# Kernel tuning notes

Hardware: AMD Instinct MI355X
Metric: run time of the kernel (lower is better)

## Reference

```python
import jax, jax.numpy as jnp
import numpy as np
from jax import lax

FILTERS = 256
KERNEL = 1
BATCH, T, D = 16, 2048, 512


def conv1d_same(x, w, b):
    # x: [B, T, Cin], w: [K, Cin, Cout], b: [Cout]
    y = lax.conv_general_dilated(
        x, w, window_strides=(1,), padding='SAME',
        dimension_numbers=('NWC', 'WIO', 'NWC'))
    return y + b


def setup_inputs() -> dict:
    key = jax.random.key(0)
    ks = jax.random.split(key, 5)
    inputs = jax.random.normal(ks[0], (BATCH, T, D), dtype=jnp.float32)
    # Glorot-ish init for conv kernels
    W_qkv = jax.random.normal(ks[1], (KERNEL, D, 3 * FILTERS), dtype=jnp.float32) * (1.0 / np.sqrt(D))
    b_qkv = jnp.zeros((3 * FILTERS,), dtype=jnp.float32)
    W_out = jax.random.normal(ks[2], (KERNEL, FILTERS, D), dtype=jnp.float32) * (1.0 / np.sqrt(FILTERS))
    b_out = jnp.zeros((D,), dtype=jnp.float32)
    return {"inputs": inputs, "W_qkv": W_qkv, "b_qkv": b_qkv, "W_out": W_out, "b_out": b_out}


def reference(inputs, W_qkv, b_qkv, W_out, b_out):
    # QKV projection: conv1d(kernel=1) == pointwise linear, kept general via conv
    qkv = conv1d_same(inputs, W_qkv, b_qkv)          # [B, T, 3F]
    q, k, v = jnp.split(qkv, 3, axis=-1)             # each [B, T, F]
    scale = jnp.sqrt(jnp.asarray(FILTERS, dtype=q.dtype))
    score = jnp.einsum('btf,bsf->bts', q, k) / scale  # [B, T, T]
    attn = jax.nn.softmax(score, axis=-1)
    context = jnp.einsum('bts,bsf->btf', attn, v)    # [B, T, F]
    output = conv1d_same(context, W_out, b_out)      # [B, T, D]
    return inputs + output
```

## Files before the change

kernel.cpp:

```cpp
#include <hip/hip_runtime.h>

typedef __bf16 bf16_t;
typedef __attribute__((ext_vector_type(8))) __bf16 bf16x8;
typedef __attribute__((ext_vector_type(4))) __bf16 bf16x4;
typedef __attribute__((ext_vector_type(4))) float f32x4;

#define GLL16(gsrc, ldst)                                                                   \
  __builtin_amdgcn_global_load_lds(                                                         \
      (const __attribute__((address_space(1))) unsigned int*)(gsrc),                        \
      (__attribute__((address_space(3))) unsigned int*)(ldst), 16, 0, 0)

#define BATCH 16
#define TT    2048
#define DD    512
#define FF    256
#define MTOT  (BATCH * TT)

__global__ __launch_bounds__(256) void cast_x_kernel(const float* __restrict__ x,
                                                     bf16_t* __restrict__ xb, int n4) {
  int stride = gridDim.x * blockDim.x;
  for (int i = blockIdx.x * blockDim.x + threadIdx.x; i < n4; i += stride) {
    float4 v = ((const float4*)x)[i];
    bf16x4 o;
    o[0] = (bf16_t)v.x; o[1] = (bf16_t)v.y; o[2] = (bf16_t)v.z; o[3] = (bf16_t)v.w;
    ((bf16x4*)xb)[i] = o;
  }
}

__global__ __launch_bounds__(256) void cast_w_kernel(const float* __restrict__ Wqkv,
                                                     const float* __restrict__ Wout,
                                                     bf16_t* __restrict__ WqkvT,
                                                     bf16_t* __restrict__ WoutT) {
  int t = blockIdx.x * blockDim.x + threadIdx.x;
  if (t < 768 * 512) {
    int n = t >> 9, k = t & 511;
    WqkvT[t] = (bf16_t)Wqkv[k * 768 + n];
  } else {
    int t2 = t - 768 * 512;
    if (t2 < 512 * 256) {
      int n = t2 >> 8, k = t2 & 255;
      WoutT[t2] = (bf16_t)Wout[k * 512 + n];
    }
  }
}

__global__ __launch_bounds__(256) void gemm_qkv_kernel(const bf16_t* __restrict__ A,
                                                       const bf16_t* __restrict__ Bt,
                                                       const float* __restrict__ bias,
                                                       bf16_t* __restrict__ Qo,
                                                       bf16_t* __restrict__ Ko,
                                                       bf16_t* __restrict__ Vt) {
  __shared__ __align__(16) bf16_t Al[2][128 * 32];
  __shared__ __align__(16) bf16_t Bl[2][128 * 32];
  const int tid = threadIdx.x;
  const int l = tid & 63, w = tid >> 6;
  const int g = l >> 4, r = l & 15;
  const int wm = w >> 1, wn = w & 1;
  const int m0 = blockIdx.y * 128;
  const int n0 = blockIdx.x * 128;
  const int lda = 512, ldb = 512;
  const bf16_t* Abase = A + (size_t)m0 * lda;
  const bf16_t* Bbase = Bt + (size_t)n0 * ldb;

  f32x4 acc[4][4] = {};

  auto stage = [&](int kt, int bufi) {
    const int k0 = kt * 32;
#pragma unroll
    for (int rnd = 0; rnd < 2; ++rnd) {
      int idx = rnd * 256 + tid;
      int row = idx >> 2, d = idx & 3;
      int sc = d ^ ((row >> 1) & 3);
      GLL16(Abase + row * lda + k0 + sc * 8, &Al[bufi][idx * 8]);
    }
#pragma unroll
    for (int rnd = 0; rnd < 2; ++rnd) {
      int idx = rnd * 256 + tid;
      int row = idx >> 2, d = idx & 3;
      int sc = d ^ ((row >> 1) & 3);
      GLL16(Bbase + row * ldb + k0 + sc * 8, &Bl[bufi][idx * 8]);
    }
  };

  stage(0, 0);
  __syncthreads();
  int buf = 0;
  const int NK = 512 / 32;
  for (int kt = 0; kt < NK; ++kt) {
    if (kt + 1 < NK) stage(kt + 1, buf ^ 1);
    bf16x8 af[4], bfr[4];
#pragma unroll
    for (int mi = 0; mi < 4; ++mi) {
      int row = wm * 64 + mi * 16 + r;
      int cc = g ^ ((row >> 1) & 3);
      af[mi] = *(const bf16x8*)&Al[buf][row * 32 + cc * 8];
    }
#pragma unroll
    for (int ni = 0; ni < 4; ++ni) {
      int row = wn * 64 + ni * 16 + r;
      int cc = g ^ ((row >> 1) & 3);
      bfr[ni] = *(const bf16x8*)&Bl[buf][row * 32 + cc * 8];
    }
#pragma unroll
    for (int mi = 0; mi < 4; ++mi)
#pragma unroll
      for (int ni = 0; ni < 4; ++ni)
        acc[mi][ni] = __builtin_amdgcn_mfma_f32_16x16x32_bf16(af[mi], bfr[ni], acc[mi][ni], 0, 0, 0);
    __syncthreads();
    buf ^= 1;
  }

  const int qsel = n0 >> 8;
#pragma unroll
  for (int mi = 0; mi < 4; ++mi) {
    int row0 = m0 + wm * 64 + mi * 16 + g * 4;
#pragma unroll
    for (int ni = 0; ni < 4; ++ni) {
      int col = n0 + wn * 64 + ni * 16 + r;
      float bv = bias[col];
      int cl = col & 255;
      if (qsel == 2) {
        bf16x4 pk;
#pragma unroll
        for (int i = 0; i < 4; ++i) pk[i] = (bf16_t)(acc[mi][ni][i] + bv);
        int b = row0 >> 11, t0 = row0 & 2047;
        *(bf16x4*)&Vt[((size_t)(b * 256 + cl)) * 2048 + t0] = pk;
      } else {
        bf16_t* dst = (qsel == 0) ? Qo : Ko;
#pragma unroll
        for (int i = 0; i < 4; ++i)
          dst[(size_t)(row0 + i) * 256 + cl] = (bf16_t)(acc[mi][ni][i] + bv);
      }
    }
  }
}

__global__ __launch_bounds__(512, 2) void attn_kernel(const bf16_t* __restrict__ Q,
                                                      const bf16_t* __restrict__ K,
                                                      const bf16_t* __restrict__ Vt,
                                                      bf16_t* __restrict__ ctx) {
  __shared__ __align__(16) bf16_t Kl[64 * 256];
  __shared__ __align__(16) bf16_t Vl[256 * 64];
  __shared__ __align__(16) bf16_t Pl[8][16 * 72];
  const int tid = threadIdx.x;
  const int l = tid & 63, w = tid >> 6;
  const int g = l >> 4, r = l & 15;
  const int b = blockIdx.y;
  const int q0 = blockIdx.x * 128 + w * 16;
  const bf16_t* Kb = K + ((size_t)b * TT) * 256;
  const bf16_t* Vb = Vt + (size_t)b * 256 * TT;

  bf16x8 qf[8];
  const bf16_t* Qrow = Q + ((size_t)(b * TT) + q0 + r) * 256;
#pragma unroll
  for (int kf = 0; kf < 8; ++kf) qf[kf] = *(const bf16x8*)(Qrow + kf * 32 + g * 8);

  f32x4 cacc[16] = {};
  float m_run = -3.0e38f, l_run = 0.0f;

  for (int kv0 = 0; kv0 < TT; kv0 += 64) {
    __syncthreads();
#pragma unroll
    for (int rnd = 0; rnd < 4; ++rnd) {
      int idx = rnd * 512 + tid;
      int row = idx >> 5, d = idx & 31;
      int sc = d ^ (row & 7);
      GLL16(Kb + (size_t)(kv0 + row) * 256 + sc * 8, &Kl[idx * 8]);
    }
#pragma unroll
    for (int rnd = 0; rnd < 4; ++rnd) {
      int idx = rnd * 512 + tid;
      int row = idx >> 3, d = idx & 7;
      int sc = d ^ (row & 7);
      GLL16(Vb + (size_t)row * TT + kv0 + sc * 8, &Vl[idx * 8]);
    }
    __syncthreads();

    f32x4 st[4] = {};
#pragma unroll
    for (int kf = 0; kf < 8; ++kf) {
#pragma unroll
      for (int kvf = 0; kvf < 4; ++kvf) {
        int row = kvf * 16 + r;
        int c = kf * 4 + g;
        bf16x8 kfr = *(const bf16x8*)&Kl[row * 256 + ((c ^ (row & 7)) * 8)];
        st[kvf] = __builtin_amdgcn_mfma_f32_16x16x32_bf16(kfr, qf[kf], st[kvf], 0, 0, 0);
      }
    }

    float tmax = -3.0e38f;
    float s[4][4];
#pragma unroll
    for (int kvf = 0; kvf < 4; ++kvf)
#pragma unroll
      for (int i = 0; i < 4; ++i) {
        s[kvf][i] = st[kvf][i] * 0.0625f;
        tmax = fmaxf(tmax, s[kvf][i]);
      }
    tmax = fmaxf(tmax, __shfl_xor(tmax, 16));
    tmax = fmaxf(tmax, __shfl_xor(tmax, 32));
    float mnew = fmaxf(m_run, tmax);
    float alpha = __expf(m_run - mnew);
    float psum = 0.0f;
#pragma unroll
    for (int kvf = 0; kvf < 4; ++kvf) {
      bf16x4 pk;
#pragma unroll
      for (int i = 0; i < 4; ++i) {
        float p = __expf(s[kvf][i] - mnew);
        psum += p;
        pk[i] = (bf16_t)p;
      }
      *(bf16x4*)&Pl[w][r * 72 + kvf * 16 + g * 4] = pk;
    }
    psum += __shfl_xor(psum, 16);
    psum += __shfl_xor(psum, 32);
    l_run = l_run * alpha + psum;
    m_run = mnew;
#pragma unroll
    for (int fc = 0; fc < 16; ++fc)
#pragma unroll
      for (int i = 0; i < 4; ++i) cacc[fc][i] *= alpha;

#pragma unroll
    for (int kk = 0; kk < 2; ++kk) {
      bf16x8 pf = *(const bf16x8*)&Pl[w][r * 72 + kk * 32 + g * 8];
#pragma unroll
      for (int fc = 0; fc < 16; ++fc) {
        int row = fc * 16 + r;
        int c = kk * 4 + g;
        bf16x8 vf = *(const bf16x8*)&Vl[row * 64 + ((c ^ (row & 7)) * 8)];
        cacc[fc] = __builtin_amdgcn_mfma_f32_16x16x32_bf16(vf, pf, cacc[fc], 0, 0, 0);
      }
    }
  }

  float inv = 1.0f / l_run;
  bf16_t* crow = ctx + ((size_t)(b * TT) + q0 + r) * 256;
#pragma unroll
  for (int fc = 0; fc < 16; ++fc) {
    bf16x4 pk;
#pragma unroll
    for (int i = 0; i < 4; ++i) pk[i] = (bf16_t)(cacc[fc][i] * inv);
    *(bf16x4*)(crow + fc * 16 + g * 4) = pk;
  }
}

__global__ __launch_bounds__(256) void gemm_out_kernel(const bf16_t* __restrict__ A,
                                                       const bf16_t* __restrict__ Bt,
                                                       const float* __restrict__ bias,
                                                       const float* __restrict__ X,
                                                       float* __restrict__ Out) {
  __shared__ __align__(16) bf16_t Al[2][128 * 32];
  __shared__ __align__(16) bf16_t Bl[2][128 * 32];
  const int tid = threadIdx.x;
  const int l = tid & 63, w = tid >> 6;
  const int g = l >> 4, r = l & 15;
  const int wm = w >> 1, wn = w & 1;
  const int m0 = blockIdx.y * 128;
  const int n0 = blockIdx.x * 128;
  const int lda = 256, ldb = 256;
  const bf16_t* Abase = A + (size_t)m0 * lda;
  const bf16_t* Bbase = Bt + (size_t)n0 * ldb;

  f32x4 acc[4][4] = {};

  auto stage = [&](int kt, int bufi) {
    const int k0 = kt * 32;
#pragma unroll
    for (int rnd = 0; rnd < 2; ++rnd) {
      int idx = rnd * 256 + tid;
      int row = idx >> 2, d = idx & 3;
      int sc = d ^ ((row >> 1) & 3);
      GLL16(Abase + row * lda + k0 + sc * 8, &Al[bufi][idx * 8]);
    }
#pragma unroll
    for (int rnd = 0; rnd < 2; ++rnd) {
      int idx = rnd * 256 + tid;
      int row = idx >> 2, d = idx & 3;
      int sc = d ^ ((row >> 1) & 3);
      GLL16(Bbase + row * ldb + k0 + sc * 8, &Bl[bufi][idx * 8]);
    }
  };

  stage(0, 0);
  __syncthreads();
  int buf = 0;
  const int NK = 256 / 32;
  for (int kt = 0; kt < NK; ++kt) {
    if (kt + 1 < NK) stage(kt + 1, buf ^ 1);
    bf16x8 af[4], bfr[4];
#pragma unroll
    for (int mi = 0; mi < 4; ++mi) {
      int row = wm * 64 + mi * 16 + r;
      int cc = g ^ ((row >> 1) & 3);
      af[mi] = *(const bf16x8*)&Al[buf][row * 32 + cc * 8];
    }
#pragma unroll
    for (int ni = 0; ni < 4; ++ni) {
      int row = wn * 64 + ni * 16 + r;
      int cc = g ^ ((row >> 1) & 3);
      bfr[ni] = *(const bf16x8*)&Bl[buf][row * 32 + cc * 8];
    }
#pragma unroll
    for (int mi = 0; mi < 4; ++mi)
#pragma unroll
      for (int ni = 0; ni < 4; ++ni)
        acc[mi][ni] = __builtin_amdgcn_mfma_f32_16x16x32_bf16(af[mi], bfr[ni], acc[mi][ni], 0, 0, 0);
    __syncthreads();
    buf ^= 1;
  }

#pragma unroll
  for (int mi = 0; mi < 4; ++mi) {
    int row0 = m0 + wm * 64 + mi * 16 + g * 4;
#pragma unroll
    for (int ni = 0; ni < 4; ++ni) {
      int col = n0 + wn * 64 + ni * 16 + r;
      float bv = bias[col];
#pragma unroll
      for (int i = 0; i < 4; ++i) {
        size_t off = (size_t)(row0 + i) * 512 + col;
        Out[off] = acc[mi][ni][i] + bv + X[off];
      }
    }
  }
}

extern "C" void kernel_launch(void* const* d_in, const int* in_sizes, int n_in,
                              void* d_out, int out_size, void* d_ws, size_t ws_size,
                              hipStream_t stream) {
  const float* X    = (const float*)d_in[0];
  const float* Wqkv = (const float*)d_in[1];
  const float* bqkv = (const float*)d_in[2];
  const float* Wout = (const float*)d_in[3];
  const float* bout = (const float*)d_in[4];
  float* out = (float*)d_out;

  char* ws = (char*)d_ws;
  bf16_t* Xbf   = (bf16_t*)ws;
  bf16_t* ctx   = Xbf;
  bf16_t* WqkvT = (bf16_t*)(ws + 33554432);
  bf16_t* WoutT = (bf16_t*)(ws + 34340864);
  bf16_t* Qb    = (bf16_t*)(ws + 34603008);
  bf16_t* Kb    = (bf16_t*)(ws + 51380224);
  bf16_t* Vt    = (bf16_t*)(ws + 68157440);

  cast_x_kernel<<<2048, 256, 0, stream>>>(X, Xbf, (MTOT * DD) / 4);
  cast_w_kernel<<<2048, 256, 0, stream>>>(Wqkv, Wout, WqkvT, WoutT);
  gemm_qkv_kernel<<<dim3(6, 256), 256, 0, stream>>>(Xbf, WqkvT, bqkv, Qb, Kb, Vt);
  attn_kernel<<<dim3(16, 16), 512, 0, stream>>>(Qb, Kb, Vt, ctx);
  gemm_out_kernel<<<dim3(4, 256), 256, 0, stream>>>(ctx, WoutT, bout, X, out);
}
```

Baseline: 334.2 us.

## Double-buffer attention K/V loads, lazy softmax rescale, XCD-aware block remap

```diff
diff --git a/kernel.cpp b/kernel.cpp
--- a/kernel.cpp
+++ b/kernel.cpp
@@ -56,8 +56,10 @@
   const int l = tid & 63, w = tid >> 6;
   const int g = l >> 4, r = l & 15;
   const int wm = w >> 1, wn = w & 1;
-  const int m0 = blockIdx.y * 128;
-  const int n0 = blockIdx.x * 128;
+  const int lin = blockIdx.x;
+  const int wid = (lin & 7) * 192 + (lin >> 3);
+  const int m0 = (wid / 6) * 128;
+  const int n0 = (wid % 6) * 128;
   const int lda = 512, ldb = 512;
   const bf16_t* Abase = A + (size_t)m0 * lda;
   const bf16_t* Bbase = Bt + (size_t)n0 * ldb;
@@ -139,14 +141,16 @@
                                                       const bf16_t* __restrict__ K,
                                                       const bf16_t* __restrict__ Vt,
                                                       bf16_t* __restrict__ ctx) {
-  __shared__ __align__(16) bf16_t Kl[64 * 256];
-  __shared__ __align__(16) bf16_t Vl[256 * 64];
-  __shared__ __align__(16) bf16_t Pl[8][16 * 72];
+  __shared__ __align__(16) bf16_t Kl[2][64 * 256];
+  __shared__ __align__(16) bf16_t Vl[2][256 * 64];
+  __shared__ __align__(16) bf16_t Pl[8][16 * 64];
   const int tid = threadIdx.x;
   const int l = tid & 63, w = tid >> 6;
   const int g = l >> 4, r = l & 15;
-  const int b = blockIdx.y;
-  const int q0 = blockIdx.x * 128 + w * 16;
+  const int lin = blockIdx.x;
+  const int wid = (lin & 7) * 32 + (lin >> 3);
+  const int b = wid >> 4;
+  const int q0 = (wid & 15) * 128 + w * 16;
   const bf16_t* Kb = K + ((size_t)b * TT) * 256;
   const bf16_t* Vb = Vt + (size_t)b * 256 * TT;
 
@@ -158,23 +162,29 @@
   f32x4 cacc[16] = {};
   float m_run = -3.0e38f, l_run = 0.0f;
 
-  for (int kv0 = 0; kv0 < TT; kv0 += 64) {
-    __syncthreads();
+  auto stage = [&](int kv0, int bi) {
 #pragma unroll
     for (int rnd = 0; rnd < 4; ++rnd) {
       int idx = rnd * 512 + tid;
       int row = idx >> 5, d = idx & 31;
       int sc = d ^ (row & 7);
-      GLL16(Kb + (size_t)(kv0 + row) * 256 + sc * 8, &Kl[idx * 8]);
+      GLL16(Kb + (size_t)(kv0 + row) * 256 + sc * 8, &Kl[bi][idx * 8]);
     }
 #pragma unroll
     for (int rnd = 0; rnd < 4; ++rnd) {
       int idx = rnd * 512 + tid;
       int row = idx >> 3, d = idx & 7;
       int sc = d ^ (row & 7);
-      GLL16(Vb + (size_t)row * TT + kv0 + sc * 8, &Vl[idx * 8]);
-    }
-    __syncthreads();
+      GLL16(Vb + (size_t)row * TT + kv0 + sc * 8, &Vl[bi][idx * 8]);
+    }
+  };
+
+  stage(0, 0);
+  __syncthreads();
+  int buf = 0;
+
+  for (int kv0 = 0; kv0 < TT; kv0 += 64) {
+    if (kv0 + 64 < TT) stage(kv0 + 64, buf ^ 1);
 
     f32x4 st[4] = {};
 #pragma unroll
@@ -183,7 +193,7 @@
       for (int kvf = 0; kvf < 4; ++kvf) {
         int row = kvf * 16 + r;
         int c = kf * 4 + g;
-        bf16x8 kfr = *(const bf16x8*)&Kl[row * 256 + ((c ^ (row & 7)) * 8)];
+        bf16x8 kfr = *(const bf16x8*)&Kl[buf][row * 256 + ((c ^ (row & 7)) * 8)];
         st[kvf] = __builtin_amdgcn_mfma_f32_16x16x32_bf16(kfr, qf[kf], st[kvf], 0, 0, 0);
       }
     }
@@ -199,40 +209,47 @@
       }
     tmax = fmaxf(tmax, __shfl_xor(tmax, 16));
     tmax = fmaxf(tmax, __shfl_xor(tmax, 32));
-    float mnew = fmaxf(m_run, tmax);
-    float alpha = __expf(m_run - mnew);
+    if (!__all(tmax - m_run <= 8.0f)) {
+      float mnew = fmaxf(m_run, tmax);
+      float alpha = __expf(m_run - mnew);
+      l_run *= alpha;
+#pragma unroll
+      for (int fc = 0; fc < 16; ++fc)
+#pragma unroll
+        for (int i = 0; i < 4; ++i) cacc[fc][i] *= alpha;
+      m_run = mnew;
+    }
     float psum = 0.0f;
 #pragma unroll
     for (int kvf = 0; kvf < 4; ++kvf) {
       bf16x4 pk;
 #pragma unroll
       for (int i = 0; i < 4; ++i) {
-        float p = __expf(s[kvf][i] - mnew);
+        float p = __expf(s[kvf][i] - m_run);
         psum += p;
         pk[i] = (bf16_t)p;
       }
-      *(bf16x4*)&Pl[w][r * 72 + kvf * 16 + g * 4] = pk;
+      int widx = r * 64 + ((((kvf * 2 + (g >> 1)) ^ (r & 7)) << 3) | ((g & 1) * 4));
+      *(bf16x4*)&Pl[w][widx] = pk;
     }
     psum += __shfl_xor(psum, 16);
     psum += __shfl_xor(psum, 32);
-    l_run = l_run * alpha + psum;
-    m_run = mnew;
-#pragma unroll
-    for (int fc = 0; fc < 16; ++fc)
-#pragma unroll
-      for (int i = 0; i < 4; ++i) cacc[fc][i] *= alpha;
+    l_run += psum;
 
 #pragma unroll
     for (int kk = 0; kk < 2; ++kk) {
-      bf16x8 pf = *(const bf16x8*)&Pl[w][r * 72 + kk * 32 + g * 8];
+      bf16x8 pf = *(const bf16x8*)&Pl[w][r * 64 + (((kk * 4 + g) ^ (r & 7)) << 3)];
 #pragma unroll
       for (int fc = 0; fc < 16; ++fc) {
         int row = fc * 16 + r;
         int c = kk * 4 + g;
-        bf16x8 vf = *(const bf16x8*)&Vl[row * 64 + ((c ^ (row & 7)) * 8)];
+        bf16x8 vf = *(const bf16x8*)&Vl[buf][row * 64 + ((c ^ (row & 7)) * 8)];
         cacc[fc] = __builtin_amdgcn_mfma_f32_16x16x32_bf16(vf, pf, cacc[fc], 0, 0, 0);
       }
     }
+
+    __syncthreads();
+    buf ^= 1;
   }
 
   float inv = 1.0f / l_run;
@@ -257,8 +274,10 @@
   const int l = tid & 63, w = tid >> 6;
   const int g = l >> 4, r = l & 15;
   const int wm = w >> 1, wn = w & 1;
-  const int m0 = blockIdx.y * 128;
-  const int n0 = blockIdx.x * 128;
+  const int lin = blockIdx.x;
+  const int wid = (lin & 7) * 128 + (lin >> 3);
+  const int m0 = (wid >> 2) * 128;
+  const int n0 = (wid & 3) * 128;
   const int lda = 256, ldb = 256;
   const bf16_t* Abase = A + (size_t)m0 * lda;
   const bf16_t* Bbase = Bt + (size_t)n0 * ldb;
@@ -348,7 +367,7 @@
 
   cast_x_kernel<<<2048, 256, 0, stream>>>(X, Xbf, (MTOT * DD) / 4);
   cast_w_kernel<<<2048, 256, 0, stream>>>(Wqkv, Wout, WqkvT, WoutT);
-  gemm_qkv_kernel<<<dim3(6, 256), 256, 0, stream>>>(Xbf, WqkvT, bqkv, Qb, Kb, Vt);
-  attn_kernel<<<dim3(16, 16), 512, 0, stream>>>(Qb, Kb, Vt, ctx);
-  gemm_out_kernel<<<dim3(4, 256), 256, 0, stream>>>(ctx, WoutT, bout, X, out);
-}
+  gemm_qkv_kernel<<<1536, 256, 0, stream>>>(Xbf, WqkvT, bqkv, Qb, Kb, Vt);
+  attn_kernel<<<256, 512, 0, stream>>>(Qb, Kb, Vt, ctx);
+  gemm_out_kernel<<<1024, 256, 0, stream>>>(ctx, WoutT, bout, X, out);
+}
```

New measurement: 315.6 us. -5.6%, faster.
